# Kernel optimization log

Measured on AMD Instinct MI355X. Metric: run time of the kernel, lower is better.

The kernel has to match this reference:

```python
import jax, jax.numpy as jnp
import numpy as np

B, T, DS, N, DR, H, DF, NK, HID = 4, 1024, 1024, 16, 256, 4, 1024, 3, 128
K_VALUES = (1, 2, 4)  # k_values for max_k=4


def _ln(x, scale, bias):
    mu = jnp.mean(x, axis=-1, keepdims=True)
    var = jnp.var(x, axis=-1, keepdims=True)
    return (x - mu) * jax.lax.rsqrt(var + 1e-5) * scale + bias


def setup_inputs() -> dict:
    key = jax.random.key(0)
    ks = jax.random.split(key, 16)
    p = lambda k, shp: 0.02 * jax.random.normal(k, shp, dtype=jnp.float32)
    return {
        "s": jax.random.normal(ks[0], (B, T, DS), dtype=jnp.float32),
        "r": jax.random.normal(ks[1], (B, T, N, DR), dtype=jnp.float32),
        # DifficultyEstimator MLP (d_s -> 128 -> 3 k-logits)
        "Wd1": p(ks[2], (DS, HID)), "bd1": jnp.zeros((HID,), jnp.float32),
        "Wd2": p(ks[3], (HID, NK)), "bd2": jnp.zeros((NK,), jnp.float32),
        # SlotAllocator (r -> hidden -> 1, plus surface projection)
        "Wa1": p(ks[4], (DR, HID)), "ba1": jnp.zeros((HID,), jnp.float32),
        "Wa2": p(ks[5], (HID, 1)), "ba2": jnp.zeros((1,), jnp.float32),
        "Ws": p(ks[6], (DS, 1)),
        # ReasoningStream: masked slot self-attention + FFN
        "ln1_s": jnp.ones((DR,), jnp.float32), "ln1_b": jnp.zeros((DR,), jnp.float32),
        "Wq": p(ks[7], (DR, DR)), "Wk": p(ks[8], (DR, DR)),
        "Wv": p(ks[9], (DR, DR)), "Wo": p(ks[10], (DR, DR)),
        "ln2_s": jnp.ones((DR,), jnp.float32), "ln2_b": jnp.zeros((DR,), jnp.float32),
        "Wf1": p(ks[11], (DR, DF)), "bf1": jnp.zeros((DF,), jnp.float32),
        "Wf2": p(ks[12], (DF, DR)), "bf2": jnp.zeros((DR,), jnp.float32),
    }


def _reasoning_step(r, mask, ln1_s, ln1_b, Wq, Wk, Wv, Wo, ln2_s, ln2_b, Wf1, bf1, Wf2, bf2):
    # one masked update of the per-position slot set: (B,T,N,DR)
    Dh = DR // H
    h = _ln(r, ln1_s, ln1_b)
    q = (h @ Wq).reshape(*h.shape[:-1], H, Dh)
    k = (h @ Wk).reshape(*h.shape[:-1], H, Dh)
    v = (h @ Wv).reshape(*h.shape[:-1], H, Dh)
    scores = jnp.einsum("btnhd,btmhd->bthnm", q, k) / jnp.sqrt(jnp.float32(Dh))
    attn = jax.nn.softmax(scores, axis=-1)
    o = jnp.einsum("bthnm,btmhd->btnhd", attn, v).reshape(r.shape) @ Wo
    r = r + mask * o
    h2 = _ln(r, ln2_s, ln2_b)
    ffn = jax.nn.gelu(h2 @ Wf1 + bf1) @ Wf2 + bf2
    return r + mask * ffn


def reference(s, r, Wd1, bd1, Wd2, bd2, Wa1, ba1, Wa2, ba2, Ws,
              ln1_s, ln1_b, Wq, Wk, Wv, Wo, ln2_s, ln2_b, Wf1, bf1, Wf2, bf2):
    # SlotAllocator: per-position per-slot soft mask (B,T,N,1)
    slot_mask = jax.nn.sigmoid(
        (jax.nn.relu(r @ Wa1 + ba1) @ Wa2 + ba2) + (s @ Ws)[:, :, None, :]
    )
    # DifficultyEstimator: k logits / weights per position (B,T,3)
    k_logits = jax.nn.relu(s @ Wd1 + bd1) @ Wd2 + bd2
    probs = jax.nn.softmax(k_logits, axis=-1)
    k_weights = probs
    # routing balance loss: mse of mean probs vs uniform
    mean_probs = probs.mean(axis=(0, 1))
    routing_loss = jnp.mean((mean_probs - 1.0 / NK) ** 2)
    k_tensor = jnp.asarray(K_VALUES, dtype=s.dtype)
    mean_k = (probs * k_tensor).sum(axis=-1).mean()
    # _combine_adaptive_reasoning (training path): run max_k steps, keep
    # candidates at k in K_VALUES, weighted combine per position.
    step_params = (ln1_s, ln1_b, Wq, Wk, Wv, Wo, ln2_s, ln2_b, Wf1, bf1, Wf2, bf2)
    candidates = []
    r_step = r
    for step in range(1, max(K_VALUES) + 1):
        r_step = _reasoning_step(r_step, slot_mask, *step_params)
        if step in K_VALUES:
            candidates.append(r_step)
    stacked = jnp.stack(candidates, axis=2)  # (B,T,3,N,DR)
    r_out = (k_weights[..., None, None] * stacked).sum(axis=2)
    return r_out, routing_loss, mean_k
```

## Files before the change

kernel.cpp:

```cpp
#include <hip/hip_runtime.h>
#include <hip/hip_bf16.h>
#include <math.h>


#define NPOS 4096
#define R_ELEMS 16777216ull
#define NB 384

typedef __attribute__((ext_vector_type(8))) short short8;
typedef __attribute__((ext_vector_type(4))) float f32x4;

#define MF(a, b, c) __builtin_amdgcn_mfma_f32_16x16x32_bf16(a, b, c, 0, 0, 0)

__device__ __forceinline__ short bf16rne(float f) {
  union { float f; unsigned u; } v; v.f = f;
  unsigned r = v.u + 0x7FFFu + ((v.u >> 16) & 1u);
  return (short)(r >> 16);
}

__device__ __forceinline__ short bf16c(float f) {
  __hip_bfloat16 h = __float2bfloat16(f);
  return *reinterpret_cast<short*>(&h);
}

__device__ __forceinline__ float fast_gelu(float x) {
  float x2 = x * x;
  float z = 0.7978845608028654f * x * (1.f + 0.044715f * x2);
  float e = __expf(2.f * z);
  float t = 1.f - 2.f * __builtin_amdgcn_rcpf(e + 1.f);
  return 0.5f * x * (1.f + t);
}

__global__ void pack_weight(const float* __restrict__ W, short* __restrict__ P,
                            int K, int N) {
  int id = blockIdx.x * 256 + threadIdx.x;
  int KC = K >> 5, T = N >> 4;
  if (id >= T * KC * 64) return;
  int l = id & 63, kc = (id >> 6) % KC, t = id / (64 * KC);
  int g = l >> 4, n = l & 15;
  short8 o;
#pragma unroll
  for (int jj = 0; jj < 8; jj++) {
    int k = 32 * kc + 4 * g + (jj & 3) + 16 * (jj >> 2);
    o[jj] = bf16rne(W[(size_t)k * N + 16 * t + n]);
  }
  *(short8*)(P + (size_t)id * 8) = o;
}

__global__ void pack_stream(const float* __restrict__ Wq, const float* __restrict__ Wk,
                            const float* __restrict__ Wv, const float* __restrict__ Wo,
                            const float* __restrict__ Wf1, const float* __restrict__ Wf2,
                            short* __restrict__ S) {
  int id = blockIdx.x * 256 + threadIdx.x;
  int f = id >> 6, lane = id & 63;
  if (f >= 1536) return;
  const float* W; int ldN, t, kc;
  if (f < 512) {
    int head = f >> 7, rem = f & 127;
    if (rem < 96) {
      int mat = rem / 32, r2 = rem % 32;
      t = 4 * head + (r2 >> 3);
      kc = r2 & 7; ldN = 256;
      W = (mat == 0) ? Wq : (mat == 1) ? Wk : Wv;
    } else {
      int r2 = rem - 96;
      int ch = r2 >> 4, floc = r2 & 15;
      t = ch * 8 + (floc >> 1);
      kc = 2 * head + (floc & 1);
      ldN = 256; W = Wo;
    }
  } else {
    int gg = f - 512, hc = gg / 32, r2 = gg % 32;
    if (r2 < 16) { W = Wf1; ldN = 1024; t = 2 * hc + (r2 >> 3); kc = r2 & 7; }
    else         { W = Wf2; ldN = 256;  t = r2 - 16;            kc = hc;    }
  }
  int g = lane >> 4, n = lane & 15;
  short8 o;
#pragma unroll
  for (int jj = 0; jj < 8; jj++) {
    int k = 32 * kc + 4 * g + (jj & 3) + 16 * (jj >> 2);
    o[jj] = bf16rne(W[(size_t)k * ldN + 16 * t + n]);
  }
  *(short8*)(S + (size_t)f * 512 + lane * 8) = o;
}

__device__ __forceinline__ short8 ldfrag(const short* __restrict__ P, int t, int kc,
                                         int KC, int lane) {
  return *(const short8*)(P + ((size_t)((t * KC + kc) * 64 + lane) << 3));
}

__global__ void init_accum_kernel(float* accum) {
  if (threadIdx.x < 4) accum[threadIdx.x] = 0.f;
}

__global__ void sproj_kernel(const float* __restrict__ s, const float* __restrict__ Ws,
                             float* __restrict__ sproj) {
  int p = blockIdx.x, tid = threadIdx.x;
  const float* row = s + (size_t)p * 1024;
  float sum = 0.f;
#pragma unroll
  for (int k0 = 0; k0 < 1024; k0 += 256) sum += row[k0 + tid] * Ws[k0 + tid];
#pragma unroll
  for (int m = 1; m < 64; m <<= 1) sum += __shfl_xor(sum, m, 64);
  __shared__ float red[4];
  if ((tid & 63) == 0) red[tid >> 6] = sum;
  __syncthreads();
  if (tid == 0) sproj[p] = red[0] + red[1] + red[2] + red[3];
}

__global__ void difficulty_mfma(const float* __restrict__ s, const short* __restrict__ PWd1,
                                const float* __restrict__ bd1, const float* __restrict__ Wd2,
                                const float* __restrict__ bd2, float* __restrict__ probsv,
                                float* __restrict__ accum) {
  int tid = threadIdx.x;
  int wave = tid >> 6, lane = tid & 63, n = lane & 15, g = lane >> 4;
  int p0 = (blockIdx.x * 4 + wave) * 16;
  const float* sg = s + (size_t)(p0 + n) * 1024;
  f32x4 ha[8];
  const f32x4 Z = {0.f, 0.f, 0.f, 0.f};
#pragma unroll
  for (int t = 0; t < 8; t++) ha[t] = Z;
  for (int kc = 0; kc < 32; kc++) {
    f32x4 x0 = *(const f32x4*)(sg + 32 * kc + 4 * g);
    f32x4 x1 = *(const f32x4*)(sg + 32 * kc + 16 + 4 * g);
    short8 sb;
#pragma unroll
    for (int c = 0; c < 4; c++) { sb[c] = bf16c(x0[c]); sb[c + 4] = bf16c(x1[c]); }
#pragma unroll
    for (int t = 0; t < 8; t++) ha[t] = MF(ldfrag(PWd1, t, kc, 32, lane), sb, ha[t]);
  }
  float v0 = 0.f, v1 = 0.f, v2 = 0.f;
#pragma unroll
  for (int t = 0; t < 8; t++)
#pragma unroll
    for (int c = 0; c < 4; c++) {
      int hid = 16 * t + 4 * g + c;
      float u = fmaxf(ha[t][c] + bd1[hid], 0.f);
      v0 += u * Wd2[hid * 3 + 0];
      v1 += u * Wd2[hid * 3 + 1];
      v2 += u * Wd2[hid * 3 + 2];
    }
  v0 += __shfl_xor(v0, 16, 64); v0 += __shfl_xor(v0, 32, 64);
  v1 += __shfl_xor(v1, 16, 64); v1 += __shfl_xor(v1, 32, 64);
  v2 += __shfl_xor(v2, 16, 64); v2 += __shfl_xor(v2, 32, 64);
  if (g == 0) {
    float l0 = v0 + bd2[0], l1 = v1 + bd2[1], l2 = v2 + bd2[2];
    float mx = fmaxf(l0, fmaxf(l1, l2));
    float e0 = __expf(l0 - mx), e1 = __expf(l1 - mx), e2 = __expf(l2 - mx);
    float inv = 1.f / (e0 + e1 + e2);
    float p0v = e0 * inv, p1v = e1 * inv, p2v = e2 * inv;
    int p = p0 + n;
    probsv[p * 3 + 0] = p0v; probsv[p * 3 + 1] = p1v; probsv[p * 3 + 2] = p2v;
    atomicAdd(accum + 0, p0v);
    atomicAdd(accum + 1, p1v);
    atomicAdd(accum + 2, p2v);
    atomicAdd(accum + 3, p0v * 1.f + p1v * 2.f + p2v * 4.f);
  }
}

__global__ void slot_mask_mfma(const float* __restrict__ r, const short* __restrict__ PWa1,
                               const float* __restrict__ ba1, const float* __restrict__ Wa2,
                               const float* __restrict__ ba2, const float* __restrict__ sproj,
                               float* __restrict__ mask) {
  int tid = threadIdx.x;
  int wave = tid >> 6, lane = tid & 63, n = lane & 15, g = lane >> 4;
  int p = blockIdx.x * 4 + wave;
  const float* rsg = r + (size_t)p * 4096 + n * 256;
  short8 rb[8];
#pragma unroll
  for (int kc = 0; kc < 8; kc++) {
    f32x4 x0 = *(const f32x4*)(rsg + 32 * kc + 4 * g);
    f32x4 x1 = *(const f32x4*)(rsg + 32 * kc + 16 + 4 * g);
    short8 o;
#pragma unroll
    for (int c = 0; c < 4; c++) { o[c] = bf16c(x0[c]); o[c + 4] = bf16c(x1[c]); }
    rb[kc] = o;
  }
  f32x4 ha[8];
  const f32x4 Z = {0.f, 0.f, 0.f, 0.f};
#pragma unroll
  for (int t = 0; t < 8; t++) ha[t] = Z;
#pragma unroll
  for (int kc = 0; kc < 8; kc++)
#pragma unroll
    for (int t = 0; t < 8; t++) ha[t] = MF(ldfrag(PWa1, t, kc, 8, lane), rb[kc], ha[t]);
  float v = 0.f;
#pragma unroll
  for (int t = 0; t < 8; t++)
#pragma unroll
    for (int c = 0; c < 4; c++) {
      int hid = 16 * t + 4 * g + c;
      v += fmaxf(ha[t][c] + ba1[hid], 0.f) * Wa2[hid];
    }
  v += __shfl_xor(v, 16, 64);
  v += __shfl_xor(v, 32, 64);
  if (g == 0) mask[p * 16 + n] = 1.f / (1.f + __expf(-(v + ba2[0] + sproj[p])));
}

__global__ __launch_bounds__(256, 2) void reason_all(
    const float* __restrict__ r_src, const float* __restrict__ maskg,
    const float* __restrict__ probsv, float* __restrict__ outp,
    const short* __restrict__ Wstream,
    const float* __restrict__ ln1s, const float* __restrict__ ln1b,
    const float* __restrict__ ln2s, const float* __restrict__ ln2b,
    const float* __restrict__ bf1g, const float* __restrict__ bf2g) {
  __shared__ __align__(16) short Wbuf[4 * 8192];
  __shared__ __align__(16) float P_ln1s[256], P_ln1b[256], P_ln2s[256], P_ln2b[256];
  __shared__ __align__(16) float P_bf1[1024], P_bf2[256];
  const int tid = threadIdx.x;
  P_ln1s[tid] = ln1s[tid]; P_ln1b[tid] = ln1b[tid];
  P_ln2s[tid] = ln2s[tid]; P_ln2b[tid] = ln2b[tid];
  P_bf2[tid] = bf2g[tid];
  for (int i = tid; i < 1024; i += 256) P_bf1[i] = bf1g[i];
  __syncthreads();

  const int wave = tid >> 6, lane = tid & 63;
  const int n = lane & 15, g = lane >> 4;
  const int pA = blockIdx.x * 8 + wave * 2, pB = pA + 1;
  const size_t baseA = (size_t)pA * 4096, baseB = (size_t)pB * 4096;
  const f32x4 Z = {0.f, 0.f, 0.f, 0.f};

  auto stage_issue = [&](int c) {
    const short* gs = Wstream + (size_t)(c % 96) * 8192 + wave * 2048 + lane * 8;
    short* ld = (short*)Wbuf + (c & 3) * 8192 + wave * 2048;
#pragma unroll
    for (int i = 0; i < 4; ++i)
      __builtin_amdgcn_global_load_lds(
          (const __attribute__((address_space(1))) void*)(gs + i * 512),
          (__attribute__((address_space(3))) void*)(ld + i * 512), 16, 0, 0);
  };
  stage_issue(0); stage_issue(1); stage_issue(2);

  f32x4 rA0[8], rA1[8], rB0[8], rB1[8];
  {
    const float* ra = r_src + baseA + n * 256;
    const float* rb = r_src + baseB + n * 256;
#pragma unroll
    for (int kc = 0; kc < 8; kc++) {
      rA0[kc] = *(const f32x4*)(ra + 32 * kc + 4 * g);
      rA1[kc] = *(const f32x4*)(ra + 32 * kc + 16 + 4 * g);
      rB0[kc] = *(const f32x4*)(rb + 32 * kc + 4 * g);
      rB1[kc] = *(const f32x4*)(rb + 32 * kc + 16 + 4 * g);
    }
  }
  const float maskA = maskg[pA * 16 + n];
  const float maskB = maskg[pB * 16 + n];

  int cidx = 0;
  auto boundary = [&]() -> const short* {
    int c = cidx++;
    if (c <= NB - 3)
      asm volatile("s_waitcnt vmcnt(8) lgkmcnt(0)\ns_barrier" ::: "memory");
    else if (c == NB - 2)
      asm volatile("s_waitcnt vmcnt(4) lgkmcnt(0)\ns_barrier" ::: "memory");
    else
      asm volatile("s_waitcnt vmcnt(0) lgkmcnt(0)\ns_barrier" ::: "memory");
    __builtin_amdgcn_sched_barrier(0);
    if (c + 3 < NB) stage_issue(c + 3);
    return &Wbuf[(c & 3) * 8192];
  };
#define FRAG(Bp, i) (*(const short8*)((Bp) + (i) * 512 + lane * 8))

  short8 hA[8], hB[8];
  auto do_ln = [&](const f32x4* r0, const f32x4* r1, const float* sc,
                   const float* bi, short8* h) {
    float sum = 0.f, sq = 0.f;
#pragma unroll
    for (int kc = 0; kc < 8; kc++)
#pragma unroll
      for (int c = 0; c < 4; c++) {
        sum += r0[kc][c] + r1[kc][c];
        sq += r0[kc][c] * r0[kc][c] + r1[kc][c] * r1[kc][c];
      }
    sum += __shfl_xor(sum, 16, 64); sq += __shfl_xor(sq, 16, 64);
    sum += __shfl_xor(sum, 32, 64); sq += __shfl_xor(sq, 32, 64);
    float mu = sum * (1.f / 256.f);
    float inv = rsqrtf(sq * (1.f / 256.f) - mu * mu + 1e-5f);
#pragma unroll
    for (int kc = 0; kc < 8; kc++) {
      f32x4 s0 = *(const f32x4*)&sc[32 * kc + 4 * g];
      f32x4 b0 = *(const f32x4*)&bi[32 * kc + 4 * g];
      f32x4 s1 = *(const f32x4*)&sc[32 * kc + 16 + 4 * g];
      f32x4 b1 = *(const f32x4*)&bi[32 * kc + 16 + 4 * g];
      short8 hh;
#pragma unroll
      for (int c = 0; c < 4; c++) {
        hh[c]     = bf16c((r0[kc][c] - mu) * inv * s0[c] + b0[c]);
        hh[c + 4] = bf16c((r1[kc][c] - mu) * inv * s1[c] + b1[c]);
      }
      h[kc] = hh;
    }
  };

#pragma unroll 1
  for (int sidx = 0; sidx < 4; ++sidx) {
    do_ln(rA0, rA1, P_ln1s, P_ln1b, hA);
    do_ln(rB0, rB1, P_ln1s, P_ln1b, hB);

#pragma unroll 1
    for (int hh = 0; hh < 4; ++hh) {
      short8 qbA[2], qbB[2], kbA[2], kbB[2];
#pragma unroll
      for (int tp = 0; tp < 2; ++tp) {
        const short* Bp = boundary();
        f32x4 a0A = Z, a1A = Z, a0B = Z, a1B = Z;
        __builtin_amdgcn_s_setprio(1);
#pragma unroll
        for (int kc = 0; kc < 8; kc++) {
          short8 fr = FRAG(Bp, kc);
          a0A = MF(fr, hA[kc], a0A); a0B = MF(fr, hB[kc], a0B);
        }
#pragma unroll
        for (int kc = 0; kc < 8; kc++) {
          short8 fr = FRAG(Bp, 8 + kc);
          a1A = MF(fr, hA[kc], a1A); a1B = MF(fr, hB[kc], a1B);
        }
        __builtin_amdgcn_s_setprio(0);
        short8 xA, xB;
#pragma unroll
        for (int jj = 0; jj < 8; jj++) {
          xA[jj] = bf16c(jj < 4 ? a0A[jj & 3] : a1A[jj & 3]);
          xB[jj] = bf16c(jj < 4 ? a0B[jj & 3] : a1B[jj & 3]);
        }
        qbA[tp] = xA; qbB[tp] = xB;
      }
#pragma unroll
      for (int tp = 0; tp < 2; ++tp) {
        const short* Bp = boundary();
        f32x4 a0A = Z, a1A = Z, a0B = Z, a1B = Z;
        __builtin_amdgcn_s_setprio(1);
#pragma unroll
        for (int kc = 0; kc < 8; kc++) {
          short8 fr = FRAG(Bp, kc);
          a0A = MF(fr, hA[kc], a0A); a0B = MF(fr, hB[kc], a0B);
        }
#pragma unroll
        for (int kc = 0; kc < 8; kc++) {
          short8 fr = FRAG(Bp, 8 + kc);
          a1A = MF(fr, hA[kc], a1A); a1B = MF(fr, hB[kc], a1B);
        }
        __builtin_amdgcn_s_setprio(0);
        short8 xA, xB;
#pragma unroll
        for (int jj = 0; jj < 8; jj++) {
          xA[jj] = bf16c(jj < 4 ? a0A[jj & 3] : a1A[jj & 3]);
          xB[jj] = bf16c(jj < 4 ? a0B[jj & 3] : a1B[jj & 3]);
        }
        kbA[tp] = xA; kbB[tp] = xB;
      }
      short8 pbA, pbB;
      {
        f32x4 sc1 = Z;
        sc1 = MF(kbA[0], qbA[0], sc1);
        sc1 = MF(kbA[1], qbA[1], sc1);
#pragma unroll
        for (int c = 0; c < 4; c++) sc1[c] *= 0.125f;
        float mx = fmaxf(fmaxf(sc1[0], sc1[1]), fmaxf(sc1[2], sc1[3]));
        mx = fmaxf(mx, __shfl_xor(mx, 16, 64));
        mx = fmaxf(mx, __shfl_xor(mx, 32, 64));
        float e0 = __expf(sc1[0] - mx), e1 = __expf(sc1[1] - mx);
        float e2 = __expf(sc1[2] - mx), e3 = __expf(sc1[3] - mx);
        float sm = e0 + e1 + e2 + e3;
        sm += __shfl_xor(sm, 16, 64);
        sm += __shfl_xor(sm, 32, 64);
        float isv = __builtin_amdgcn_rcpf(sm);
        pbA[0] = bf16c(e0 * isv); pbA[1] = bf16c(e1 * isv);
        pbA[2] = bf16c(e2 * isv); pbA[3] = bf16c(e3 * isv);
        pbA[4] = 0; pbA[5] = 0; pbA[6] = 0; pbA[7] = 0;
      }
      {
        f32x4 sc1 = Z;
        sc1 = MF(kbB[0], qbB[0], sc1);
        sc1 = MF(kbB[1], qbB[1], sc1);
#pragma unroll
        for (int c = 0; c < 4; c++) sc1[c] *= 0.125f;
        float mx = fmaxf(fmaxf(sc1[0], sc1[1]), fmaxf(sc1[2], sc1[3]));
        mx = fmaxf(mx, __shfl_xor(mx, 16, 64));
        mx = fmaxf(mx, __shfl_xor(mx, 32, 64));
        float e0 = __expf(sc1[0] - mx), e1 = __expf(sc1[1] - mx);
        float e2 = __expf(sc1[2] - mx), e3 = __expf(sc1[3] - mx);
        float sm = e0 + e1 + e2 + e3;
        sm += __shfl_xor(sm, 16, 64);
        sm += __shfl_xor(sm, 32, 64);
        float isv = __builtin_amdgcn_rcpf(sm);
        pbB[0] = bf16c(e0 * isv); pbB[1] = bf16c(e1 * isv);
        pbB[2] = bf16c(e2 * isv); pbB[3] = bf16c(e3 * isv);
        pbB[4] = 0; pbB[5] = 0; pbB[6] = 0; pbB[7] = 0;
      }
      short8 osA[2], osB[2];
#pragma unroll
      for (int tp = 0; tp < 2; ++tp) {
        const short* Bp = boundary();
        f32x4 v0A = Z, v1A = Z, v0B = Z, v1B = Z;
        __builtin_amdgcn_s_setprio(1);
#pragma unroll
        for (int kc = 0; kc < 8; kc++) {
          short8 fr = FRAG(Bp, kc);
          v0A = MF(hA[kc], fr, v0A); v0B = MF(hB[kc], fr, v0B);
        }
#pragma unroll
        for (int kc = 0; kc < 8; kc++) {
          short8 fr = FRAG(Bp, 8 + kc);
          v1A = MF(hA[kc], fr, v1A); v1B = MF(hB[kc], fr, v1B);
        }
        __builtin_amdgcn_s_setprio(0);
        short8 vb0A, vb1A, vb0B, vb1B;
#pragma unroll
        for (int c = 0; c < 4; c++) {
          vb0A[c] = bf16c(v0A[c]); vb1A[c] = bf16c(v1A[c]);
          vb0B[c] = bf16c(v0B[c]); vb1B[c] = bf16c(v1B[c]);
          vb0A[c + 4] = 0; vb1A[c + 4] = 0; vb0B[c + 4] = 0; vb1B[c + 4] = 0;
        }
        f32x4 oh0A = MF(vb0A, pbA, Z), oh1A = MF(vb1A, pbA, Z);
        f32x4 oh0B = MF(vb0B, pbB, Z), oh1B = MF(vb1B, pbB, Z);
        short8 yA, yB;
#pragma unroll
        for (int jj = 0; jj < 8; jj++) {
          yA[jj] = bf16c(maskA * (jj < 4 ? oh0A[jj & 3] : oh1A[jj & 3]));
          yB[jj] = bf16c(maskB * (jj < 4 ? oh0B[jj & 3] : oh1B[jj & 3]));
        }
        osA[tp] = yA; osB[tp] = yB;
      }
#pragma unroll
      for (int ch = 0; ch < 2; ++ch) {
        const short* Bp = boundary();
        __builtin_amdgcn_s_setprio(1);
#pragma unroll
        for (int tloc = 0; tloc < 8; ++tloc) {
          short8 f0 = FRAG(Bp, 2 * tloc), f1 = FRAG(Bp, 2 * tloc + 1);
          int kk = ch * 4 + (tloc >> 1);
          if ((tloc & 1) == 0) {
            rA0[kk] = MF(f0, osA[0], rA0[kk]); rA0[kk] = MF(f1, osA[1], rA0[kk]);
            rB0[kk] = MF(f0, osB[0], rB0[kk]); rB0[kk] = MF(f1, osB[1], rB0[kk]);
          } else {
            rA1[kk] = MF(f0, osA[0], rA1[kk]); rA1[kk] = MF(f1, osA[1], rA1[kk]);
            rB1[kk] = MF(f0, osB[0], rB1[kk]); rB1[kk] = MF(f1, osB[1], rB1[kk]);
          }
        }
        __builtin_amdgcn_s_setprio(0);
      }
    }

    do_ln(rA0, rA1, P_ln2s, P_ln2b, hA);
    do_ln(rB0, rB1, P_ln2s, P_ln2b, hB);
#pragma unroll 1
    for (int hc = 0; hc < 32; hc++) {
      f32x4 t0A = Z, t1A = Z, t0B = Z, t1B = Z;
      {
        const short* Bp = boundary();
        __builtin_amdgcn_s_setprio(1);
#pragma unroll
        for (int kc = 0; kc < 8; kc++) {
          short8 fr = FRAG(Bp, kc);
          t0A = MF(fr, hA[kc], t0A); t0B = MF(fr, hB[kc], t0B);
        }
#pragma unroll
        for (int kc = 0; kc < 8; kc++) {
          short8 fr = FRAG(Bp, 8 + kc);
          t1A = MF(fr, hA[kc], t1A); t1B = MF(fr, hB[kc], t1B);
        }
        __builtin_amdgcn_s_setprio(0);
      }
      f32x4 u0 = *(const f32x4*)&P_bf1[32 * hc + 4 * g];
      f32x4 u1 = *(const f32x4*)&P_bf1[32 * hc + 16 + 4 * g];
      short8 hbbA, hbbB;
#pragma unroll
      for (int c = 0; c < 4; c++) {
        hbbA[c]     = bf16c(maskA * fast_gelu(t0A[c] + u0[c]));
        hbbA[c + 4] = bf16c(maskA * fast_gelu(t1A[c] + u1[c]));
        hbbB[c]     = bf16c(maskB * fast_gelu(t0B[c] + u0[c]));
        hbbB[c + 4] = bf16c(maskB * fast_gelu(t1B[c] + u1[c]));
      }
      {
        const short* Bp = boundary();
        __builtin_amdgcn_s_setprio(1);
#pragma unroll
        for (int tt = 0; tt < 8; tt++) {
          short8 f0 = FRAG(Bp, 2 * tt), f1 = FRAG(Bp, 2 * tt + 1);
          rA0[tt] = MF(f0, hbbA, rA0[tt]); rB0[tt] = MF(f0, hbbB, rB0[tt]);
          rA1[tt] = MF(f1, hbbA, rA1[tt]); rB1[tt] = MF(f1, hbbB, rB1[tt]);
        }
        __builtin_amdgcn_s_setprio(0);
      }
    }
#pragma unroll
    for (int kc = 0; kc < 8; kc++) {
      f32x4 b0 = *(const f32x4*)&P_bf2[32 * kc + 4 * g];
      f32x4 b1 = *(const f32x4*)&P_bf2[32 * kc + 16 + 4 * g];
#pragma unroll
      for (int c = 0; c < 4; c++) {
        rA0[kc][c] += maskA * b0[c]; rA1[kc][c] += maskA * b1[c];
        rB0[kc][c] += maskB * b0[c]; rB1[kc][c] += maskB * b1[c];
      }
    }

    if (sidx == 0) {
      float wa = probsv[pA * 3 + 0], wb = probsv[pB * 3 + 0];
      float* oa = outp + baseA + n * 256;
      float* ob2 = outp + baseB + n * 256;
#pragma unroll
      for (int kc = 0; kc < 8; kc++) {
        f32x4 xa0, xa1, xb0, xb1;
#pragma unroll
        for (int c = 0; c < 4; c++) {
          xa0[c] = wa * rA0[kc][c]; xa1[c] = wa * rA1[kc][c];
          xb0[c] = wb * rB0[kc][c]; xb1[c] = wb * rB1[kc][c];
        }
        *(f32x4*)(oa + 32 * kc + 4 * g) = xa0;
        *(f32x4*)(oa + 32 * kc + 16 + 4 * g) = xa1;
        *(f32x4*)(ob2 + 32 * kc + 4 * g) = xb0;
        *(f32x4*)(ob2 + 32 * kc + 16 + 4 * g) = xb1;
      }
    } else if (sidx == 1 || sidx == 3) {
      int ci = (sidx == 1) ? 1 : 2;
      float wa = probsv[pA * 3 + ci], wb = probsv[pB * 3 + ci];
      float* oa = outp + baseA + n * 256;
      float* ob2 = outp + baseB + n * 256;
#pragma unroll
      for (int kc = 0; kc < 8; kc++) {
        f32x4 xa0 = *(f32x4*)(oa + 32 * kc + 4 * g);
        f32x4 xa1 = *(f32x4*)(oa + 32 * kc + 16 + 4 * g);
        f32x4 xb0 = *(f32x4*)(ob2 + 32 * kc + 4 * g);
        f32x4 xb1 = *(f32x4*)(ob2 + 32 * kc + 16 + 4 * g);
#pragma unroll
        for (int c = 0; c < 4; c++) {
          xa0[c] += wa * rA0[kc][c]; xa1[c] += wa * rA1[kc][c];
          xb0[c] += wb * rB0[kc][c]; xb1[c] += wb * rB1[kc][c];
        }
        *(f32x4*)(oa + 32 * kc + 4 * g) = xa0;
        *(f32x4*)(oa + 32 * kc + 16 + 4 * g) = xa1;
        *(f32x4*)(ob2 + 32 * kc + 4 * g) = xb0;
        *(f32x4*)(ob2 + 32 * kc + 16 + 4 * g) = xb1;
      }
    }
  }
}

__global__ void finalize_kernel(const float* __restrict__ accum, float* __restrict__ dst) {
  const float inv = 1.f / 4096.f;
  float m0 = accum[0] * inv, m1 = accum[1] * inv, m2 = accum[2] * inv;
  const float u = 1.f / 3.f;
  float d0 = m0 - u, d1 = m1 - u, d2 = m2 - u;
  dst[0] = (d0 * d0 + d1 * d1 + d2 * d2) * (1.f / 3.f);
  dst[1] = accum[3] * inv;
}

extern "C" void kernel_launch(void* const* d_in, const int* in_sizes, int n_in,
                              void* d_out, int out_size, void* d_ws, size_t ws_size,
                              hipStream_t stream) {
  const float* s    = (const float*)d_in[0];
  const float* r    = (const float*)d_in[1];
  const float* Wd1  = (const float*)d_in[2];
  const float* bd1  = (const float*)d_in[3];
  const float* Wd2  = (const float*)d_in[4];
  const float* bd2  = (const float*)d_in[5];
  const float* Wa1  = (const float*)d_in[6];
  const float* ba1  = (const float*)d_in[7];
  const float* Wa2  = (const float*)d_in[8];
  const float* ba2  = (const float*)d_in[9];
  const float* Wsp  = (const float*)d_in[10];
  const float* ln1s = (const float*)d_in[11];
  const float* ln1b = (const float*)d_in[12];
  const float* Wq   = (const float*)d_in[13];
  const float* Wk   = (const float*)d_in[14];
  const float* Wv   = (const float*)d_in[15];
  const float* Wo   = (const float*)d_in[16];
  const float* ln2s = (const float*)d_in[17];
  const float* ln2b = (const float*)d_in[18];
  const float* Wf1  = (const float*)d_in[19];
  const float* bf1  = (const float*)d_in[20];
  const float* Wf2  = (const float*)d_in[21];
  const float* bf2  = (const float*)d_in[22];

  float* out = (float*)d_out;
  float* wsf = (float*)d_ws;
  float* mask   = wsf;
  float* sproj  = wsf + 65536;
  float* probsv = wsf + 65536 + 4096;
  float* accum  = wsf + 65536 + 4096 + 12288;
  short* pk     = (short*)(wsf + 131072);
  short* Wstream = pk;
  short* PWa1    = pk + 786432;
  short* PWd1    = pk + 819200;

  pack_stream<<<384, 256, 0, stream>>>(Wq, Wk, Wv, Wo, Wf1, Wf2, Wstream);
  pack_weight<<<16, 256, 0, stream>>>(Wa1, PWa1, 256, 128);
  pack_weight<<<64, 256, 0, stream>>>(Wd1, PWd1, 1024, 128);

  init_accum_kernel<<<1, 64, 0, stream>>>(accum);
  sproj_kernel<<<NPOS, 256, 0, stream>>>(s, Wsp, sproj);
  difficulty_mfma<<<64, 256, 0, stream>>>(s, PWd1, bd1, Wd2, bd2, probsv, accum);
  slot_mask_mfma<<<NPOS / 4, 256, 0, stream>>>(r, PWa1, ba1, Wa2, ba2, sproj, mask);

  reason_all<<<NPOS / 8, 256, 0, stream>>>(r, mask, probsv, out, Wstream,
                                           ln1s, ln1b, ln2s, ln2b, bf1, bf2);

  finalize_kernel<<<1, 1, 0, stream>>>(accum, out + R_ELEMS);
}
```

Baseline: 604.2 us.

## Give each wave a private double-buffered weight stream and drop block barriers

Replaces the block-shared 4-stage LDS weight ring, which needed an s_barrier at every chunk, with per-wave private double buffers. Each wave streams every weight chunk itself into its own 8 KB slot, using half-size chunks and only vmcnt waits, so waves no longer synchronise with each other. The cost is that global/L2 weight traffic is four times higher, since each wave loads all weights instead of a quarter, and the prefetch depth drops from three stages to one.

```diff
diff --git a/kernel.cpp b/kernel.cpp
--- a/kernel.cpp
+++ b/kernel.cpp
@@ -5,7 +5,8 @@
 
 #define NPOS 4096
 #define R_ELEMS 16777216ull
-#define NB 384
+#define CPS 192
+#define NCHUNK_TOT 768
 
 typedef __attribute__((ext_vector_type(8))) short short8;
 typedef __attribute__((ext_vector_type(4))) float f32x4;
@@ -204,7 +205,7 @@
     const float* __restrict__ ln1s, const float* __restrict__ ln1b,
     const float* __restrict__ ln2s, const float* __restrict__ ln2b,
     const float* __restrict__ bf1g, const float* __restrict__ bf2g) {
-  __shared__ __align__(16) short Wbuf[4 * 8192];
+  __shared__ __align__(16) short Wbuf[4 * 2 * 4096];
   __shared__ __align__(16) float P_ln1s[256], P_ln1b[256], P_ln2s[256], P_ln2b[256];
   __shared__ __align__(16) float P_bf1[1024], P_bf2[256];
   const int tid = threadIdx.x;
@@ -219,17 +220,18 @@
   const int pA = blockIdx.x * 8 + wave * 2, pB = pA + 1;
   const size_t baseA = (size_t)pA * 4096, baseB = (size_t)pB * 4096;
   const f32x4 Z = {0.f, 0.f, 0.f, 0.f};
-
-  auto stage_issue = [&](int c) {
-    const short* gs = Wstream + (size_t)(c % 96) * 8192 + wave * 2048 + lane * 8;
-    short* ld = (short*)Wbuf + (c & 3) * 8192 + wave * 2048;
-#pragma unroll
-    for (int i = 0; i < 4; ++i)
+  short* const myBuf = (short*)Wbuf + wave * 8192;
+
+  auto stage_issue = [&](int slc, int par) {
+    const short* gs = Wstream + (size_t)slc * 4096 + lane * 8;
+    short* ld = myBuf + par * 4096;
+#pragma unroll
+    for (int i = 0; i < 8; ++i)
       __builtin_amdgcn_global_load_lds(
           (const __attribute__((address_space(1))) void*)(gs + i * 512),
           (__attribute__((address_space(3))) void*)(ld + i * 512), 16, 0, 0);
   };
-  stage_issue(0); stage_issue(1); stage_issue(2);
+  stage_issue(0, 0);
 
   f32x4 rA0[8], rA1[8], rB0[8], rB1[8];
   {
@@ -246,18 +248,20 @@
   const float maskA = maskg[pA * 16 + n];
   const float maskB = maskg[pB * 16 + n];
 
-  int cidx = 0;
+  int fc = 0, lcc = 0;
   auto boundary = [&]() -> const short* {
-    int c = cidx++;
-    if (c <= NB - 3)
-      asm volatile("s_waitcnt vmcnt(8) lgkmcnt(0)\ns_barrier" ::: "memory");
-    else if (c == NB - 2)
-      asm volatile("s_waitcnt vmcnt(4) lgkmcnt(0)\ns_barrier" ::: "memory");
-    else
-      asm volatile("s_waitcnt vmcnt(0) lgkmcnt(0)\ns_barrier" ::: "memory");
+    int nf = fc + 1;
+    int nlc = lcc + 1; if (nlc == CPS) nlc = 0;
+    if (nf < NCHUNK_TOT) {
+      stage_issue(nlc, nf & 1);
+      asm volatile("s_waitcnt vmcnt(8)" ::: "memory");
+    } else {
+      asm volatile("s_waitcnt vmcnt(0)" ::: "memory");
+    }
     __builtin_amdgcn_sched_barrier(0);
-    if (c + 3 < NB) stage_issue(c + 3);
-    return &Wbuf[(c & 3) * 8192];
+    const short* B = myBuf + (fc & 1) * 4096;
+    fc = nf; lcc = nlc;
+    return B;
   };
 #define FRAG(Bp, i) (*(const short8*)((Bp) + (i) * 512 + lane * 8))
 
@@ -302,20 +306,27 @@
       short8 qbA[2], qbB[2], kbA[2], kbB[2];
 #pragma unroll
       for (int tp = 0; tp < 2; ++tp) {
-        const short* Bp = boundary();
-        f32x4 a0A = Z, a1A = Z, a0B = Z, a1B = Z;
-        __builtin_amdgcn_s_setprio(1);
-#pragma unroll
-        for (int kc = 0; kc < 8; kc++) {
-          short8 fr = FRAG(Bp, kc);
-          a0A = MF(fr, hA[kc], a0A); a0B = MF(fr, hB[kc], a0B);
-        }
-#pragma unroll
-        for (int kc = 0; kc < 8; kc++) {
-          short8 fr = FRAG(Bp, 8 + kc);
-          a1A = MF(fr, hA[kc], a1A); a1B = MF(fr, hB[kc], a1B);
-        }
-        __builtin_amdgcn_s_setprio(0);
+        f32x4 a0A = Z, a0B = Z, a1A = Z, a1B = Z;
+        {
+          const short* Bp = boundary();
+          __builtin_amdgcn_s_setprio(1);
+#pragma unroll
+          for (int kc = 0; kc < 8; kc++) {
+            short8 fr = FRAG(Bp, kc);
+            a0A = MF(fr, hA[kc], a0A); a0B = MF(fr, hB[kc], a0B);
+          }
+          __builtin_amdgcn_s_setprio(0);
+        }
+        {
+          const short* Bp = boundary();
+          __builtin_amdgcn_s_setprio(1);
+#pragma unroll
+          for (int kc = 0; kc < 8; kc++) {
+            short8 fr = FRAG(Bp, kc);
+            a1A = MF(fr, hA[kc], a1A); a1B = MF(fr, hB[kc], a1B);
+          }
+          __builtin_amdgcn_s_setprio(0);
+        }
         short8 xA, xB;
 #pragma unroll
         for (int jj = 0; jj < 8; jj++) {
@@ -326,20 +337,27 @@
       }
 #pragma unroll
       for (int tp = 0; tp < 2; ++tp) {
-        const short* Bp = boundary();
-        f32x4 a0A = Z, a1A = Z, a0B = Z, a1B = Z;
-        __builtin_amdgcn_s_setprio(1);
-#pragma unroll
-        for (int kc = 0; kc < 8; kc++) {
-          short8 fr = FRAG(Bp, kc);
-          a0A = MF(fr, hA[kc], a0A); a0B = MF(fr, hB[kc], a0B);
-        }
-#pragma unroll
-        for (int kc = 0; kc < 8; kc++) {
-          short8 fr = FRAG(Bp, 8 + kc);
-          a1A = MF(fr, hA[kc], a1A); a1B = MF(fr, hB[kc], a1B);
-        }
-        __builtin_amdgcn_s_setprio(0);
+        f32x4 a0A = Z, a0B = Z, a1A = Z, a1B = Z;
+        {
+          const short* Bp = boundary();
+          __builtin_amdgcn_s_setprio(1);
+#pragma unroll
+          for (int kc = 0; kc < 8; kc++) {
+            short8 fr = FRAG(Bp, kc);
+            a0A = MF(fr, hA[kc], a0A); a0B = MF(fr, hB[kc], a0B);
+          }
+          __builtin_amdgcn_s_setprio(0);
+        }
+        {
+          const short* Bp = boundary();
+          __builtin_amdgcn_s_setprio(1);
+#pragma unroll
+          for (int kc = 0; kc < 8; kc++) {
+            short8 fr = FRAG(Bp, kc);
+            a1A = MF(fr, hA[kc], a1A); a1B = MF(fr, hB[kc], a1B);
+          }
+          __builtin_amdgcn_s_setprio(0);
+        }
         short8 xA, xB;
 #pragma unroll
         for (int jj = 0; jj < 8; jj++) {
@@ -390,20 +408,27 @@
       short8 osA[2], osB[2];
 #pragma unroll
       for (int tp = 0; tp < 2; ++tp) {
-        const short* Bp = boundary();
-        f32x4 v0A = Z, v1A = Z, v0B = Z, v1B = Z;
-        __builtin_amdgcn_s_setprio(1);
-#pragma unroll
-        for (int kc = 0; kc < 8; kc++) {
-          short8 fr = FRAG(Bp, kc);
-          v0A = MF(hA[kc], fr, v0A); v0B = MF(hB[kc], fr, v0B);
-        }
-#pragma unroll
-        for (int kc = 0; kc < 8; kc++) {
-          short8 fr = FRAG(Bp, 8 + kc);
-          v1A = MF(hA[kc], fr, v1A); v1B = MF(hB[kc], fr, v1B);
-        }
-        __builtin_amdgcn_s_setprio(0);
+        f32x4 v0A = Z, v0B = Z, v1A = Z, v1B = Z;
+        {
+          const short* Bp = boundary();
+          __builtin_amdgcn_s_setprio(1);
+#pragma unroll
+          for (int kc = 0; kc < 8; kc++) {
+            short8 fr = FRAG(Bp, kc);
+            v0A = MF(hA[kc], fr, v0A); v0B = MF(hB[kc], fr, v0B);
+          }
+          __builtin_amdgcn_s_setprio(0);
+        }
+        {
+          const short* Bp = boundary();
+          __builtin_amdgcn_s_setprio(1);
+#pragma unroll
+          for (int kc = 0; kc < 8; kc++) {
+            short8 fr = FRAG(Bp, kc);
+            v1A = MF(hA[kc], fr, v1A); v1B = MF(hB[kc], fr, v1B);
+          }
+          __builtin_amdgcn_s_setprio(0);
+        }
         short8 vb0A, vb1A, vb0B, vb1B;
 #pragma unroll
         for (int c = 0; c < 4; c++) {
@@ -422,14 +447,14 @@
         osA[tp] = yA; osB[tp] = yB;
       }
 #pragma unroll
-      for (int ch = 0; ch < 2; ++ch) {
+      for (int w = 0; w < 4; ++w) {
         const short* Bp = boundary();
         __builtin_amdgcn_s_setprio(1);
 #pragma unroll
-        for (int tloc = 0; tloc < 8; ++tloc) {
-          short8 f0 = FRAG(Bp, 2 * tloc), f1 = FRAG(Bp, 2 * tloc + 1);
-          int kk = ch * 4 + (tloc >> 1);
-          if ((tloc & 1) == 0) {
+        for (int m = 0; m < 4; ++m) {
+          short8 f0 = FRAG(Bp, 2 * m), f1 = FRAG(Bp, 2 * m + 1);
+          int kk = (w >> 1) * 4 + (w & 1) * 2 + (m >> 1);
+          if ((m & 1) == 0) {
             rA0[kk] = MF(f0, osA[0], rA0[kk]); rA0[kk] = MF(f1, osA[1], rA0[kk]);
             rB0[kk] = MF(f0, osB[0], rB0[kk]); rB0[kk] = MF(f1, osB[1], rB0[kk]);
           } else {
@@ -445,7 +470,7 @@
     do_ln(rB0, rB1, P_ln2s, P_ln2b, hB);
 #pragma unroll 1
     for (int hc = 0; hc < 32; hc++) {
-      f32x4 t0A = Z, t1A = Z, t0B = Z, t1B = Z;
+      f32x4 t0A = Z, t0B = Z, t1A = Z, t1B = Z;
       {
         const short* Bp = boundary();
         __builtin_amdgcn_s_setprio(1);
@@ -454,9 +479,14 @@
           short8 fr = FRAG(Bp, kc);
           t0A = MF(fr, hA[kc], t0A); t0B = MF(fr, hB[kc], t0B);
         }
+        __builtin_amdgcn_s_setprio(0);
+      }
+      {
+        const short* Bp = boundary();
+        __builtin_amdgcn_s_setprio(1);
 #pragma unroll
         for (int kc = 0; kc < 8; kc++) {
-          short8 fr = FRAG(Bp, 8 + kc);
+          short8 fr = FRAG(Bp, kc);
           t1A = MF(fr, hA[kc], t1A); t1B = MF(fr, hB[kc], t1B);
         }
         __builtin_amdgcn_s_setprio(0);
@@ -475,10 +505,21 @@
         const short* Bp = boundary();
         __builtin_amdgcn_s_setprio(1);
 #pragma unroll
-        for (int tt = 0; tt < 8; tt++) {
-          short8 f0 = FRAG(Bp, 2 * tt), f1 = FRAG(Bp, 2 * tt + 1);
-          rA0[tt] = MF(f0, hbbA, rA0[tt]); rB0[tt] = MF(f0, hbbB, rB0[tt]);
-          rA1[tt] = MF(f1, hbbA, rA1[tt]); rB1[tt] = MF(f1, hbbB, rB1[tt]);
+        for (int m = 0; m < 4; ++m) {
+          short8 f0 = FRAG(Bp, 2 * m), f1 = FRAG(Bp, 2 * m + 1);
+          rA0[m] = MF(f0, hbbA, rA0[m]); rB0[m] = MF(f0, hbbB, rB0[m]);
+          rA1[m] = MF(f1, hbbA, rA1[m]); rB1[m] = MF(f1, hbbB, rB1[m]);
+        }
+        __builtin_amdgcn_s_setprio(0);
+      }
+      {
+        const short* Bp = boundary();
+        __builtin_amdgcn_s_setprio(1);
+#pragma unroll
+        for (int m = 0; m < 4; ++m) {
+          short8 f0 = FRAG(Bp, 2 * m), f1 = FRAG(Bp, 2 * m + 1);
+          rA0[4 + m] = MF(f0, hbbA, rA0[4 + m]); rB0[4 + m] = MF(f0, hbbB, rB0[4 + m]);
+          rA1[4 + m] = MF(f1, hbbA, rA1[4 + m]); rB1[4 + m] = MF(f1, hbbB, rB1[4 + m]);
         }
         __builtin_amdgcn_s_setprio(0);
       }
```

Result: slower. 725.5 us (+20.1%).

## Read weight fragments directly from global memory instead of LDS ring buffer

Applied to the files above, without the earlier changes.

Removes the 4-deep LDS ring buffer fed by global_load_lds and its per-chunk waitcnt and barrier. Each wave now loads its MFMA weight fragments straight from global memory (L2/L1 cached) by a fixed fragment index. This drops block-wide barriers and frees 64KB of LDS, which may raise occupancy. In exchange every wave issues its own redundant global loads, the weight reads are no longer prefetched ahead of use, and load latency sits directly in the MFMA chains.

```diff
diff --git a/kernel.cpp b/kernel.cpp
--- a/kernel.cpp
+++ b/kernel.cpp
@@ -5,7 +5,6 @@
 
 #define NPOS 4096
 #define R_ELEMS 16777216ull
-#define NB 384
 
 typedef __attribute__((ext_vector_type(8))) short short8;
 typedef __attribute__((ext_vector_type(4))) float f32x4;
@@ -204,7 +203,6 @@
     const float* __restrict__ ln1s, const float* __restrict__ ln1b,
     const float* __restrict__ ln2s, const float* __restrict__ ln2b,
     const float* __restrict__ bf1g, const float* __restrict__ bf2g) {
-  __shared__ __align__(16) short Wbuf[4 * 8192];
   __shared__ __align__(16) float P_ln1s[256], P_ln1b[256], P_ln2s[256], P_ln2b[256];
   __shared__ __align__(16) float P_bf1[1024], P_bf2[256];
   const int tid = threadIdx.x;
@@ -220,16 +218,8 @@
   const size_t baseA = (size_t)pA * 4096, baseB = (size_t)pB * 4096;
   const f32x4 Z = {0.f, 0.f, 0.f, 0.f};
 
-  auto stage_issue = [&](int c) {
-    const short* gs = Wstream + (size_t)(c % 96) * 8192 + wave * 2048 + lane * 8;
-    short* ld = (short*)Wbuf + (c & 3) * 8192 + wave * 2048;
-#pragma unroll
-    for (int i = 0; i < 4; ++i)
-      __builtin_amdgcn_global_load_lds(
-          (const __attribute__((address_space(1))) void*)(gs + i * 512),
-          (__attribute__((address_space(3))) void*)(ld + i * 512), 16, 0, 0);
-  };
-  stage_issue(0); stage_issue(1); stage_issue(2);
+  const short* const Wl = Wstream + lane * 8;
+#define GF(fi) (*(const short8*)(Wl + (size_t)(fi) * 512))
 
   f32x4 rA0[8], rA1[8], rB0[8], rB1[8];
   {
@@ -245,21 +235,6 @@
   }
   const float maskA = maskg[pA * 16 + n];
   const float maskB = maskg[pB * 16 + n];
-
-  int cidx = 0;
-  auto boundary = [&]() -> const short* {
-    int c = cidx++;
-    if (c <= NB - 3)
-      asm volatile("s_waitcnt vmcnt(8) lgkmcnt(0)\ns_barrier" ::: "memory");
-    else if (c == NB - 2)
-      asm volatile("s_waitcnt vmcnt(4) lgkmcnt(0)\ns_barrier" ::: "memory");
-    else
-      asm volatile("s_waitcnt vmcnt(0) lgkmcnt(0)\ns_barrier" ::: "memory");
-    __builtin_amdgcn_sched_barrier(0);
-    if (c + 3 < NB) stage_issue(c + 3);
-    return &Wbuf[(c & 3) * 8192];
-  };
-#define FRAG(Bp, i) (*(const short8*)((Bp) + (i) * 512 + lane * 8))
 
   short8 hA[8], hB[8];
   auto do_ln = [&](const f32x4* r0, const f32x4* r1, const float* sc,
@@ -299,20 +274,20 @@
 
 #pragma unroll 1
     for (int hh = 0; hh < 4; ++hh) {
+      const int hb = hh * 128;
       short8 qbA[2], qbB[2], kbA[2], kbB[2];
 #pragma unroll
       for (int tp = 0; tp < 2; ++tp) {
-        const short* Bp = boundary();
         f32x4 a0A = Z, a1A = Z, a0B = Z, a1B = Z;
         __builtin_amdgcn_s_setprio(1);
 #pragma unroll
         for (int kc = 0; kc < 8; kc++) {
-          short8 fr = FRAG(Bp, kc);
+          short8 fr = GF(hb + tp * 16 + kc);
           a0A = MF(fr, hA[kc], a0A); a0B = MF(fr, hB[kc], a0B);
         }
 #pragma unroll
         for (int kc = 0; kc < 8; kc++) {
-          short8 fr = FRAG(Bp, 8 + kc);
+          short8 fr = GF(hb + tp * 16 + 8 + kc);
           a1A = MF(fr, hA[kc], a1A); a1B = MF(fr, hB[kc], a1B);
         }
         __builtin_amdgcn_s_setprio(0);
@@ -326,17 +301,16 @@
       }
 #pragma unroll
       for (int tp = 0; tp < 2; ++tp) {
-        const short* Bp = boundary();
         f32x4 a0A = Z, a1A = Z, a0B = Z, a1B = Z;
         __builtin_amdgcn_s_setprio(1);
 #pragma unroll
         for (int kc = 0; kc < 8; kc++) {
-          short8 fr = FRAG(Bp, kc);
+          short8 fr = GF(hb + 32 + tp * 16 + kc);
           a0A = MF(fr, hA[kc], a0A); a0B = MF(fr, hB[kc], a0B);
         }
 #pragma unroll
         for (int kc = 0; kc < 8; kc++) {
-          short8 fr = FRAG(Bp, 8 + kc);
+          short8 fr = GF(hb + 32 + tp * 16 + 8 + kc);
           a1A = MF(fr, hA[kc], a1A); a1B = MF(fr, hB[kc], a1B);
         }
         __builtin_amdgcn_s_setprio(0);
@@ -390,17 +364,16 @@
       short8 osA[2], osB[2];
 #pragma unroll
       for (int tp = 0; tp < 2; ++tp) {
-        const short* Bp = boundary();
         f32x4 v0A = Z, v1A = Z, v0B = Z, v1B = Z;
         __builtin_amdgcn_s_setprio(1);
 #pragma unroll
         for (int kc = 0; kc < 8; kc++) {
-          short8 fr = FRAG(Bp, kc);
+          short8 fr = GF(hb + 64 + tp * 16 + kc);
           v0A = MF(hA[kc], fr, v0A); v0B = MF(hB[kc], fr, v0B);
         }
 #pragma unroll
         for (int kc = 0; kc < 8; kc++) {
-          short8 fr = FRAG(Bp, 8 + kc);
+          short8 fr = GF(hb + 64 + tp * 16 + 8 + kc);
           v1A = MF(hA[kc], fr, v1A); v1B = MF(hB[kc], fr, v1B);
         }
         __builtin_amdgcn_s_setprio(0);
@@ -421,13 +394,13 @@
         }
         osA[tp] = yA; osB[tp] = yB;
       }
+      __builtin_amdgcn_s_setprio(1);
 #pragma unroll
       for (int ch = 0; ch < 2; ++ch) {
-        const short* Bp = boundary();
-        __builtin_amdgcn_s_setprio(1);
 #pragma unroll
         for (int tloc = 0; tloc < 8; ++tloc) {
-          short8 f0 = FRAG(Bp, 2 * tloc), f1 = FRAG(Bp, 2 * tloc + 1);
+          short8 f0 = GF(hb + 96 + ch * 16 + 2 * tloc);
+          short8 f1 = GF(hb + 96 + ch * 16 + 2 * tloc + 1);
           int kk = ch * 4 + (tloc >> 1);
           if ((tloc & 1) == 0) {
             rA0[kk] = MF(f0, osA[0], rA0[kk]); rA0[kk] = MF(f1, osA[1], rA0[kk]);
@@ -437,30 +410,28 @@
             rB1[kk] = MF(f0, osB[0], rB1[kk]); rB1[kk] = MF(f1, osB[1], rB1[kk]);
           }
         }
-        __builtin_amdgcn_s_setprio(0);
-      }
+      }
+      __builtin_amdgcn_s_setprio(0);
     }
 
     do_ln(rA0, rA1, P_ln2s, P_ln2b, hA);
     do_ln(rB0, rB1, P_ln2s, P_ln2b, hB);
 #pragma unroll 1
     for (int hc = 0; hc < 32; hc++) {
+      const int fb = 512 + hc * 32;
       f32x4 t0A = Z, t1A = Z, t0B = Z, t1B = Z;
-      {
-        const short* Bp = boundary();
-        __builtin_amdgcn_s_setprio(1);
-#pragma unroll
-        for (int kc = 0; kc < 8; kc++) {
-          short8 fr = FRAG(Bp, kc);
-          t0A = MF(fr, hA[kc], t0A); t0B = MF(fr, hB[kc], t0B);
-        }
-#pragma unroll
-        for (int kc = 0; kc < 8; kc++) {
-          short8 fr = FRAG(Bp, 8 + kc);
-          t1A = MF(fr, hA[kc], t1A); t1B = MF(fr, hB[kc], t1B);
-        }
-        __builtin_amdgcn_s_setprio(0);
-      }
+      __builtin_amdgcn_s_setprio(1);
+#pragma unroll
+      for (int kc = 0; kc < 8; kc++) {
+        short8 fr = GF(fb + kc);
+        t0A = MF(fr, hA[kc], t0A); t0B = MF(fr, hB[kc], t0B);
+      }
+#pragma unroll
+      for (int kc = 0; kc < 8; kc++) {
+        short8 fr = GF(fb + 8 + kc);
+        t1A = MF(fr, hA[kc], t1A); t1B = MF(fr, hB[kc], t1B);
+      }
+      __builtin_amdgcn_s_setprio(0);
       f32x4 u0 = *(const f32x4*)&P_bf1[32 * hc + 4 * g];
       f32x4 u1 = *(const f32x4*)&P_bf1[32 * hc + 16 + 4 * g];
       short8 hbbA, hbbB;
@@ -471,17 +442,15 @@
         hbbB[c]     = bf16c(maskB * fast_gelu(t0B[c] + u0[c]));
         hbbB[c + 4] = bf16c(maskB * fast_gelu(t1B[c] + u1[c]));
       }
-      {
-        const short* Bp = boundary();
-        __builtin_amdgcn_s_setprio(1);
-#pragma unroll
-        for (int tt = 0; tt < 8; tt++) {
-          short8 f0 = FRAG(Bp, 2 * tt), f1 = FRAG(Bp, 2 * tt + 1);
-          rA0[tt] = MF(f0, hbbA, rA0[tt]); rB0[tt] = MF(f0, hbbB, rB0[tt]);
-          rA1[tt] = MF(f1, hbbA, rA1[tt]); rB1[tt] = MF(f1, hbbB, rB1[tt]);
-        }
-        __builtin_amdgcn_s_setprio(0);
-      }
+      __builtin_amdgcn_s_setprio(1);
+#pragma unroll
+      for (int tt = 0; tt < 8; tt++) {
+        short8 f0 = GF(fb + 16 + 2 * tt);
+        short8 f1 = GF(fb + 16 + 2 * tt + 1);
+        rA0[tt] = MF(f0, hbbA, rA0[tt]); rB0[tt] = MF(f0, hbbB, rB0[tt]);
+        rA1[tt] = MF(f1, hbbA, rA1[tt]); rB1[tt] = MF(f1, hbbB, rB1[tt]);
+      }
+      __builtin_amdgcn_s_setprio(0);
     }
 #pragma unroll
     for (int kc = 0; kc < 8; kc++) {
```

New measurement: 1.874 ms. +210.2%, slower.
